# Kernel tuning notes

Measured on AMD Instinct MI355X. Metric: run time of the kernel, lower is better.

Reference implementation:

```python
import jax, jax.numpy as jnp
import numpy as np

E = 256; H = 8; HD = E // H
L_LEN = 300; A_LEN = 250
T = 768; B = 4
NEG = -1e9


def setup_inputs() -> dict:
    rng = jax.random.key(0)
    ks = jax.random.split(rng, 16)
    n = lambda k, s, sc=1.0: jax.random.normal(k, s, dtype=jnp.float32) * sc
    return {
        "query": n(ks[0], (T, B, E)),
        "key": n(ks[1], (T, B, E)),
        "value": n(ks[2], (T, B, E)),
        "in_proj_w": n(ks[3], (3 * E, E), 0.05),
        "in_proj_b": jnp.zeros((3 * E,), jnp.float32),
        "out_w": n(ks[4], (7, E, E), 0.05),
        "out_b": jnp.zeros((7, E), jnp.float32),
        "s_l_w": n(ks[5], (E, 4 * E), 0.05),
        "s_l_b": jnp.zeros((E,), jnp.float32),
        "s_a_w": n(ks[6], (E, 4 * E), 0.05),
        "s_a_b": jnp.zeros((E,), jnp.float32),
        "s_v_w": n(ks[7], (E, 4 * E), 0.05),
        "s_v_b": jnp.zeros((E,), jnp.float32),
        "final_w": n(ks[8], (E, E), 0.05),
        "final_b": jnp.zeros((E,), jnp.float32),
    }


def _forward(query, key, value, in_proj_w, in_proj_b, out_w, out_b,
             s_l_w, s_l_b, s_a_w, s_a_b, s_v_w, s_v_b, final_w, final_b):
    t, b, e = query.shape
    scaling = HD ** -0.5
    Wq, Wk, Wv = in_proj_w[:E], in_proj_w[E:2 * E], in_proj_w[2 * E:]
    bq, bk, bv = in_proj_b[:E], in_proj_b[E:2 * E], in_proj_b[2 * E:]
    q = (query @ Wq.T + bq) * scaling
    k = key @ Wk.T + bk
    v = value @ Wv.T + bv
    # (T, B, E) -> (B*H, T, HD)
    sh = lambda x: x.reshape(t, b * H, HD).transpose(1, 0, 2)
    q, k, v = sh(q), sh(k), sh(v)
    # shared QK^T, reused by all 7 masked branches
    scores = jnp.einsum('bth,bsh->bts', q, k)  # (B*H, T, T)
    idx = jnp.arange(t)
    seg = jnp.where(idx < L_LEN, 0, jnp.where(idx < L_LEN + A_LEN, 1, 2))

    def branch(i, mods):
        # m[j] = 1 iff position j belongs to one of the selected modalities
        m = sum((seg == s) for s in mods).astype(scores.dtype)  # (T,)
        # additive mask: in-set query attends only in-set keys; out-of-set
        # query rows get all -1e9 (uniform softmax, zeroed by row mask below)
        add = jnp.where((m[:, None] * m[None, :]) > 0, 0.0, NEG)
        w = jax.nn.softmax(scores + add, axis=-1) * m[None, :, None]
        o = jnp.einsum('bts,bsh->bth', w, v * m[None, :, None])
        o = o.transpose(1, 0, 2).reshape(t, b, e)
        return o @ out_w[i].T + out_b[i]

    attn_lav = branch(0, (0, 1, 2))
    attn_la = branch(1, (0, 1))
    attn_lv = branch(2, (0, 2))
    attn_av = branch(3, (1, 2))
    attn_l = branch(4, (0,))
    attn_a = branch(5, (1,))
    attn_v = branch(6, (2,))

    sl = jnp.concatenate([attn_lav, attn_la, attn_lv, attn_l], -1) @ s_l_w.T + s_l_b
    sa = jnp.concatenate([attn_lav, attn_la, attn_av, attn_a], -1) @ s_a_w.T + s_a_b
    sv = jnp.concatenate([attn_lav, attn_lv, attn_av, attn_v], -1) @ s_v_w.T + s_v_b
    return (sl + sa + sv) @ final_w.T + final_b


def reference(query, key, value, in_proj_w, in_proj_b, out_w, out_b,
              s_l_w, s_l_b, s_a_w, s_a_b, s_v_w, s_v_b, final_w, final_b):
    return _forward(query, key, value, in_proj_w, in_proj_b, out_w, out_b,
                    s_l_w, s_l_b, s_a_w, s_a_b, s_v_w, s_v_b, final_w, final_b)
```

## Files before the change

kernel.cpp:

```cpp
#include <hip/hip_runtime.h>
#include <hip/hip_bf16.h>

#define E 256
#define H 8
#define HD 32
#define T 768
#define B 4
#define BH 32

typedef __attribute__((ext_vector_type(8))) short bf16x8;
typedef __attribute__((ext_vector_type(4))) float f32x4;
typedef __attribute__((ext_vector_type(16))) float f32x16;

__device__ __forceinline__ float b2f(__hip_bfloat16 x) { return __bfloat162float(x); }

__device__ __forceinline__ unsigned short f2bf_u(float x) {
    __hip_bfloat16 h = __float2bfloat16(x);
    return *(unsigned short*)&h;
}
__device__ __forceinline__ float bfu2f(unsigned short u) {
    return __uint_as_float(((unsigned int)u) << 16);
}

__device__ __forceinline__ int detect_f32(const void* query) {
    const unsigned short* q = (const unsigned short*)query;
    int lane = threadIdx.x & 63;
    int bad = 0;
    #pragma unroll
    for (int i = 0; i < 4; ++i) {
        float v = bfu2f(q[lane + i * 64]);
        bad |= (!(v == v) || fabsf(v) > 1e4f) ? 1 : 0;
    }
    return __any(bad) ? 1 : 0;
}

__device__ __forceinline__ void f8_split(const float* v, bf16x8& h, bf16x8& l) {
    #pragma unroll
    for (int e = 0; e < 8; ++e) {
        unsigned short hu = f2bf_u(v[e]);
        h[e] = (short)hu;
        l[e] = (short)f2bf_u(v[e] - bfu2f(hu));
    }
}

#define MFMA3(ACC, AH, AL, BH_, BL_)                                         \
    ACC = __builtin_amdgcn_mfma_f32_16x16x32_bf16(AH, BH_, ACC, 0, 0, 0);    \
    ACC = __builtin_amdgcn_mfma_f32_16x16x32_bf16(AH, BL_, ACC, 0, 0, 0);    \
    ACC = __builtin_amdgcn_mfma_f32_16x16x32_bf16(AL, BH_, ACC, 0, 0, 0);

#define MFMA3W(ACC, AH, AL, BH_, BL_)                                        \
    ACC = __builtin_amdgcn_mfma_f32_32x32x16_bf16(AH, BH_, ACC, 0, 0, 0);    \
    ACC = __builtin_amdgcn_mfma_f32_32x32x16_bf16(AH, BL_, ACC, 0, 0, 0);    \
    ACC = __builtin_amdgcn_mfma_f32_32x32x16_bf16(AL, BH_, ACC, 0, 0, 0);

__device__ __forceinline__ bf16x8 mk8(int a, int b, int c, int d) {
    union { int i[4]; bf16x8 v; } u;
    u.i[0] = a; u.i[1] = b; u.i[2] = c; u.i[3] = d;
    return u.v;
}

__device__ __forceinline__ float ldu(const void* p, size_t i, int f32) {
    if (f32) return ((const float*)p)[i];
    return b2f(((const __hip_bfloat16*)p)[i]);
}

__device__ __forceinline__ float gsum_load(int i, int r2, int r,
                                           const void* sl, const void* sa,
                                           const void* sv, int f32)
{
    size_t base = (size_t)r2 * 1024;
    switch (i) {
        case 0: return ldu(sl, base + r, f32) + ldu(sa, base + r, f32) + ldu(sv, base + r, f32);
        case 1: return ldu(sl, base + 256 + r, f32) + ldu(sa, base + 256 + r, f32);
        case 2: return ldu(sl, base + 512 + r, f32) + ldu(sv, base + 256 + r, f32);
        case 3: return ldu(sa, base + 512 + r, f32) + ldu(sv, base + 512 + r, f32);
        case 4: return ldu(sl, base + 768 + r, f32);
        case 5: return ldu(sa, base + 768 + r, f32);
        default: return ldu(sv, base + 768 + r, f32);
    }
}

__global__ __launch_bounds__(256) void stage1_kernel(
    const void* query, const void* key, const void* value, const void* w,
    const void* sl, const void* sa, const void* sv, const void* outw,
    const void* outb, const void* slb, const void* sab, const void* svb,
    unsigned short* __restrict__ XFh, unsigned short* __restrict__ XFl,
    unsigned short* __restrict__ WFh, unsigned short* __restrict__ WFl,
    unsigned short* __restrict__ GFh, unsigned short* __restrict__ GFl,
    unsigned short* __restrict__ OWFh, unsigned short* __restrict__ OWFl,
    float* __restrict__ c0)
{
    __shared__ float red[256];
    int f32 = detect_f32(query);
    if (blockIdx.x < 1696) {
        int item = blockIdx.x * 256 + threadIdx.x;
        if (item < 294912) {
            int inp = item / 98304;
            int rem = item % 98304;
            int row = rem >> 5, kg = rem & 31;
            const void* X = (inp == 0) ? query : (inp == 1) ? key : value;
            float v[8];
            if (f32) {
                const float4* p = (const float4*)((const float*)X +
                                   (size_t)row * 256 + kg * 8);
                *(float4*)&v[0] = p[0];
                *(float4*)&v[4] = p[1];
            } else {
                #pragma unroll
                for (int j = 0; j < 8; ++j)
                    v[j] = ldu(X, (size_t)row * 256 + kg * 8 + j, 0);
            }
            bf16x8 h, l;
            f8_split(v, h, l);
            int rb = row >> 4, kb = kg >> 2;
            int lane = (row & 15) | ((kg & 3) << 4);
            size_t idx = (((size_t)(inp * 192 + rb) * 8 + kb) * 64 + lane) * 8;
            *(bf16x8*)&XFh[idx] = h;
            *(bf16x8*)&XFl[idx] = l;
        } else if (item < 319488) {
            int rem = item - 294912;
            int gc = rem >> 5, kg = rem & 31;
            float v[8];
            if (f32) {
                const float4* p = (const float4*)((const float*)w +
                                   (size_t)gc * 256 + kg * 8);
                *(float4*)&v[0] = p[0];
                *(float4*)&v[4] = p[1];
            } else {
                #pragma unroll
                for (int j = 0; j < 8; ++j)
                    v[j] = ldu(w, (size_t)gc * 256 + kg * 8 + j, 0);
            }
            bf16x8 h, l;
            f8_split(v, h, l);
            int sec = gc >> 8, c = gc & 255;
            int cb = c >> 4, kb = kg >> 2;
            int lane = (c & 15) | ((kg & 3) << 4);
            size_t idx = (((size_t)(sec * 16 + cb) * 8 + kb) * 64 + lane) * 8;
            *(bf16x8*)&WFh[idx] = h;
            *(bf16x8*)&WFl[idx] = l;
        } else if (item < 376832) {
            int rem = item - 319488;
            int i = rem >> 13;
            int rest = rem & 8191;
            int r2 = rest >> 5, kg = rest & 31;
            float v[8];
            #pragma unroll
            for (int j = 0; j < 8; ++j)
                v[j] = gsum_load(i, r2, kg * 8 + j, sl, sa, sv, f32);
            bf16x8 h, l;
            f8_split(v, h, l);
            int rb = r2 >> 4, kb = kg >> 2;
            int lane = (r2 & 15) | ((kg & 3) << 4);
            size_t idx = (((size_t)(i * 16 + rb) * 8 + kb) * 64 + lane) * 8;
            *(bf16x8*)&GFh[idx] = h;
            *(bf16x8*)&GFl[idx] = l;
        } else if (item < 434176) {
            int rem = item - 376832;
            int i = rem >> 13;
            int rest = rem & 8191;
            int kg = rest >> 8, c = rest & 255;
            float v[8];
            #pragma unroll
            for (int j = 0; j < 8; ++j)
                v[j] = ldu(outw, (size_t)i * 65536 + (kg * 8 + j) * 256 + c, f32);
            bf16x8 h, l;
            f8_split(v, h, l);
            int cb = c >> 4, kb = kg >> 2;
            int lane = (c & 15) | ((kg & 3) << 4);
            size_t idx = (((size_t)(i * 16 + cb) * 8 + kb) * 64 + lane) * 8;
            *(bf16x8*)&OWFh[idx] = h;
            *(bf16x8*)&OWFl[idx] = l;
        }
    } else {
        int r2 = blockIdx.x - 1696, m = threadIdx.x;
        float acc = 0.f;
        #pragma unroll
        for (int i = 0; i < 7; ++i)
            acc += ldu(outb, i * 256 + m, f32) * gsum_load(i, r2, m, sl, sa, sv, f32);
        red[m] = acc;
        __syncthreads();
        for (int s = 128; s > 0; s >>= 1) {
            if (m < s) red[m] += red[m + s];
            __syncthreads();
        }
        if (m == 0)
            c0[r2] = red[0] + ldu(slb, r2, f32) + ldu(sab, r2, f32) + ldu(svb, r2, f32);
    }
}

__global__ __launch_bounds__(256) void stage2_kernel(
    const unsigned short* __restrict__ XFh, const unsigned short* __restrict__ XFl,
    const unsigned short* __restrict__ WFh, const unsigned short* __restrict__ WFl,
    const void* bias, const void* query,
    float* __restrict__ qws,
    unsigned short* __restrict__ KRh, unsigned short* __restrict__ KRl,
    unsigned short* __restrict__ VFh, unsigned short* __restrict__ VFl,
    const unsigned short* __restrict__ GFh, const unsigned short* __restrict__ GFl,
    const unsigned short* __restrict__ OWFh, const unsigned short* __restrict__ OWFl,
    float* __restrict__ Mtmp,
    const float* __restrict__ c0, const void* finalw, const void* finalb,
    float* __restrict__ d0)
{
    __shared__ float red[256];
    int bxx = blockIdx.x;
    if (bxx < 2304) {
        int f32 = detect_f32(query);
        int bx = bxx % 12;
        int rb = bxx / 12;
        int sec = bx >> 2, cg = bx & 3;
        int w = threadIdx.x >> 6, lane = threadIdx.x & 63;
        int m = lane & 15, quad = lane >> 4;
        int cb = cg * 4 + w;

        const unsigned short* Ah = XFh + (((size_t)(sec * 192 + rb) * 8) * 64 + lane) * 8;
        const unsigned short* Al = XFl + (((size_t)(sec * 192 + rb) * 8) * 64 + lane) * 8;
        const unsigned short* Bh = WFh + (((size_t)(sec * 16 + cb) * 8) * 64 + lane) * 8;
        const unsigned short* Bl = WFl + (((size_t)(sec * 16 + cb) * 8) * 64 + lane) * 8;

        f32x4 acc = {};
        #pragma unroll
        for (int kb = 0; kb < 8; ++kb) {
            size_t off = (size_t)kb * 512;
            bf16x8 ah = *(const bf16x8*)(Ah + off);
            bf16x8 al = *(const bf16x8*)(Al + off);
            bf16x8 bh = *(const bf16x8*)(Bh + off);
            bf16x8 bl = *(const bf16x8*)(Bl + off);
            MFMA3(acc, ah, al, bh, bl)
        }

        int c_local = cb * 16 + m;
        float bv = ldu(bias, sec * 256 + c_local, f32);
        int h = c_local >> 5, hd = c_local & 31;

        if (sec == 0) {
            #pragma unroll
            for (int rr = 0; rr < 4; ++rr) {
                int row = rb * 16 + quad * 4 + rr;
                int t = row >> 2, b = row & 3;
                float val = (acc[rr] + bv) * 0.17677669529663687f;
                qws[((size_t)((b * H + h) * T + t)) * HD + hd] = val;
            }
        } else if (sec == 1) {
            #pragma unroll
            for (int rr = 0; rr < 4; ++rr) {
                int row = rb * 16 + quad * 4 + rr;
                int s = row >> 2, b = row & 3;
                int bh_ = b * 8 + h;
                float val = acc[rr] + bv;
                unsigned short hu = f2bf_u(val);
                unsigned short lu = f2bf_u(val - bfu2f(hu));
                size_t bi = ((size_t)bh_ * 768 + s) * 32 + hd;
                KRh[bi] = hu;
                KRl[bi] = lu;
            }
        } else {
            #pragma unroll
            for (int rr = 0; rr < 4; ++rr) {
                int row = rb * 16 + quad * 4 + rr;
                int s = row >> 2, b = row & 3;
                int bh_ = b * 8 + h;
                float val = acc[rr] + bv;
                unsigned short hu = f2bf_u(val);
                unsigned short lu = f2bf_u(val - bfu2f(hu));
                int s16 = s >> 4, hp = (s >> 3) & 1, j = s & 7;
                size_t bi = (((size_t)bh_ * 48 + s16) * 64 + hp * 32 + hd) * 8 + j;
                VFh[bi] = hu;
                VFl[bi] = lu;
            }
        }
    } else if (bxx < 2752) {
        int idx = bxx - 2304;
        int cgrp = idx & 3;
        int rb   = (idx >> 2) & 15;
        int i    = idx >> 6;
        int w = threadIdx.x >> 6, lane = threadIdx.x & 63;
        int m = lane & 15, quad = lane >> 4;
        int cb = cgrp * 4 + w;

        const unsigned short* Ah = GFh + (((size_t)(i * 16 + rb) * 8) * 64 + lane) * 8;
        const unsigned short* Al = GFl + (((size_t)(i * 16 + rb) * 8) * 64 + lane) * 8;
        const unsigned short* Bh = OWFh + (((size_t)(i * 16 + cb) * 8) * 64 + lane) * 8;
        const unsigned short* Bl = OWFl + (((size_t)(i * 16 + cb) * 8) * 64 + lane) * 8;

        f32x4 acc = {};
        #pragma unroll
        for (int kb = 0; kb < 8; ++kb) {
            size_t off = (size_t)kb * 512;
            bf16x8 ah = *(const bf16x8*)(Ah + off);
            bf16x8 al = *(const bf16x8*)(Al + off);
            bf16x8 bh = *(const bf16x8*)(Bh + off);
            bf16x8 bl = *(const bf16x8*)(Bl + off);
            MFMA3(acc, ah, al, bh, bl)
        }
        #pragma unroll
        for (int rr = 0; rr < 4; ++rr) {
            int r2 = rb * 16 + quad * 4 + rr;
            Mtmp[(size_t)i * 65536 + r2 * 256 + cb * 16 + m] = acc[rr];
        }
    } else {
        int f32 = detect_f32(query);
        int e = bxx - 2752, r = threadIdx.x;
        red[r] = c0[r] * ldu(finalw, (size_t)e * 256 + r, f32);
        __syncthreads();
        for (int s = 128; s > 0; s >>= 1) {
            if (r < s) red[r] += red[r + s];
            __syncthreads();
        }
        if (r == 0)
            d0[e] = red[0] + ldu(finalb, e, f32);
    }
}

__global__ __launch_bounds__(256, 2) void stage3_kernel(
    const float* __restrict__ qws,
    const unsigned short* __restrict__ KRh, const unsigned short* __restrict__ KRl,
    const unsigned short* __restrict__ VFh, const unsigned short* __restrict__ VFl,
    unsigned short* __restrict__ Ohi, unsigned short* __restrict__ Olo,
    const float* __restrict__ Mtmp, const void* finalw, const void* query,
    unsigned short* __restrict__ DThi, unsigned short* __restrict__ DTlo)
{
    __shared__ __align__(16) float SMEM[7104];
    int tid = threadIdx.x;

    if (blockIdx.x < 768) {
        float (*AC2)[3][32][36] = (float(*)[3][32][36])&SMEM[0];
        float (*SS2)[3][32]     = (float(*)[3][32])&SMEM[6912];
        int bid = blockIdx.x;
        int xcd = bid & 7, rr_ = bid >> 3;
        int j_ = rr_ / 24, tile = rr_ % 24;
        int bh = j_ * 8 + xcd;
        int t0 = tile * 32;
        int w = tid >> 6, lane = tid & 63;
        int ln = lane & 31, h = lane >> 5;

        bf16x8 qbh[2], qbl[2];
        {
            const float* qr = qws + ((size_t)bh * T + t0 + ln) * HD + h * 8;
            #pragma unroll
            for (int c = 0; c < 2; ++c) {
                float qv[8];
                *(float4*)&qv[0] = *(const float4*)(qr + c * 16);
                *(float4*)&qv[4] = *(const float4*)(qr + c * 16 + 4);
                f8_split(qv, qbh[c], qbl[c]);
            }
        }

        f32x16 accA = {}, accB = {};
        float ssA = 0.f, ssB = 0.f;

        for (int q = 0; q < 3; ++q) {
            int ch = w * 3 + q;
            int sbase = ch * 64;
            int route = (ch == 5) ? 1 : (ch == 4 || ch == 8) ? 2 : 0;
            int bnd = (ch == 4) ? 300 : 550;
            bool c12 = (ch == 4);

            bf16x8 kf0h[2], kf0l[2], kf1h[2], kf1l[2], vh[4], vl[4];
            #pragma unroll
            for (int st = 0; st < 2; ++st) {
                size_t krow = ((size_t)bh * 768 + sbase + st * 32 + ln) * 32 + h * 8;
                kf0h[st] = *(const bf16x8*)(KRh + krow);
                kf0l[st] = *(const bf16x8*)(KRl + krow);
                kf1h[st] = *(const bf16x8*)(KRh + krow + 16);
                kf1l[st] = *(const bf16x8*)(KRl + krow + 16);
            }
            #pragma unroll
            for (int ks = 0; ks < 4; ++ks) {
                size_t vidx = (((size_t)bh * 48 + ch * 4 + ks) * 64 + lane) * 8;
                vh[ks] = *(const bf16x8*)(VFh + vidx);
                vl[ks] = *(const bf16x8*)(VFl + vidx);
            }

            #pragma unroll
            for (int st = 0; st < 2; ++st) {
                f32x16 d = {};
                MFMA3W(d, kf0h[st], kf0l[st], qbh[0], qbl[0])
                MFMA3W(d, kf1h[st], kf1l[st], qbh[1], qbl[1])

                int PH[8], PL[8];
                #pragma unroll
                for (int p = 0; p < 8; ++p) {
                    float e0 = __expf(d[2 * p]);
                    float e1 = __expf(d[2 * p + 1]);
                    if (route == 2) {
                        int r0 = 2 * p;
                        int s0 = sbase + st * 32 + (r0 & 3) + 8 * (r0 >> 2) + 4 * h;
                        if (s0 < bnd) ssA += e0; else ssB += e0;
                        if (s0 + 1 < bnd) ssA += e1; else ssB += e1;
                    } else if (route == 1) { ssB += e0 + e1; }
                    else { ssA += e0 + e1; }
                    unsigned b0 = __float_as_uint(e0), b1 = __float_as_uint(e1);
                    float l0 = e0 - __uint_as_float(b0 & 0xffff0000u);
                    float l1 = e1 - __uint_as_float(b1 & 0xffff0000u);
                    PH[p] = (int)((b0 >> 16) | (b1 & 0xffff0000u));
                    PL[p] = (int)((__float_as_uint(l0) >> 16) |
                                  (__float_as_uint(l1) & 0xffff0000u));
                }

                #pragma unroll
                for (int ksl = 0; ksl < 2; ++ksl) {
                    int ks = st * 2 + ksl;
                    int cc = 4 * ksl;
                    bf16x8 vbh = vh[ks];
                    bf16x8 vbl = vl[ks];

                    int sh0 = __shfl_xor(PH[cc+0], 32);
                    int sh1 = __shfl_xor(PH[cc+1], 32);
                    int sh2 = __shfl_xor(PH[cc+2], 32);
                    int sh3 = __shfl_xor(PH[cc+3], 32);
                    int sl0 = __shfl_xor(PL[cc+0], 32);
                    int sl1 = __shfl_xor(PL[cc+1], 32);
                    int sl2 = __shfl_xor(PL[cc+2], 32);
                    int sl3 = __shfl_xor(PL[cc+3], 32);
                    int FH0 = h ? sh2 : PH[cc+0];
                    int FH1 = h ? sh3 : PH[cc+1];
                    int FH2 = h ? PH[cc+2] : sh0;
                    int FH3 = h ? PH[cc+3] : sh1;
                    int FL0 = h ? sl2 : PL[cc+0];
                    int FL1 = h ? sl3 : PL[cc+1];
                    int FL2 = h ? PL[cc+2] : sl0;
                    int FL3 = h ? PL[cc+3] : sl1;
                    bf16x8 feh = mk8(FH0, FH1, FH2, FH3);
                    bf16x8 fel = mk8(FL0, FL1, FL2, FL3);

                    if (route == 0)      { MFMA3W(accA, feh, fel, vbh, vbl) }
                    else if (route == 1) { MFMA3W(accB, feh, fel, vbh, vbl) }
                    else {
                        if (ks < 2)       { MFMA3W(accA, feh, fel, vbh, vbl) }
                        else if (ks == 3) { MFMA3W(accB, feh, fel, vbh, vbl) }
                        else {
                            int a0 = h ? (c12 ? FH0 : 0) : FH0;
                            int a1 = h ? (c12 ? FH1 : 0) : FH1;
                            int a2 = h ? 0 : FH2;
                            int a3 = h ? 0 : (c12 ? FH3 : 0);
                            int b0 = h ? (c12 ? 0 : FH0) : 0;
                            int b1 = h ? (c12 ? 0 : FH1) : 0;
                            int b2 = h ? FH2 : 0;
                            int b3 = h ? FH3 : (c12 ? 0 : FH3);
                            int la0 = h ? (c12 ? FL0 : 0) : FL0;
                            int la1 = h ? (c12 ? FL1 : 0) : FL1;
                            int la2 = h ? 0 : FL2;
                            int la3 = h ? 0 : (c12 ? FL3 : 0);
                            int lb0 = h ? (c12 ? 0 : FL0) : 0;
                            int lb1 = h ? (c12 ? 0 : FL1) : 0;
                            int lb2 = h ? FL2 : 0;
                            int lb3 = h ? FL3 : (c12 ? 0 : FL3);
                            bf16x8 fha = mk8(a0, a1, a2, a3), fla = mk8(la0, la1, la2, la3);
                            bf16x8 fhb = mk8(b0, b1, b2, b3), flb = mk8(lb0, lb1, lb2, lb3);
                            MFMA3W(accA, fha, fla, vbh, vbl)
                            MFMA3W(accB, fhb, flb, vbh, vbl)
                        }
                    }
                }
            }
        }

        ssA += __shfl_xor(ssA, 32);
        ssB += __shfl_xor(ssB, 32);

        int bsel = w & 1;
        f32x16 zz = {};
        f32x16 o0 = (w <= 1) ? accA : zz;
        f32x16 o1 = (w == 1) ? accB : (w == 2) ? accA : zz;
        f32x16 o2 = (w == 2) ? accB : (w == 3) ? accA : zz;
        float s0 = (w <= 1) ? ssA : 0.f;
        float s1 = (w == 1) ? ssB : (w == 2) ? ssA : 0.f;
        float s2 = (w == 2) ? ssB : (w == 3) ? ssA : 0.f;

        if (w < 2) {
            #pragma unroll
            for (int r = 0; r < 16; ++r) {
                int t = (r & 3) + 8 * (r >> 2) + 4 * h;
                AC2[bsel][0][t][ln] = o0[r];
                AC2[bsel][1][t][ln] = o1[r];
                AC2[bsel][2][t][ln] = o2[r];
            }
            if (h == 0) {
                SS2[bsel][0][ln] = s0;
                SS2[bsel][1][ln] = s1;
                SS2[bsel][2][ln] = s2;
            }
        }
        __syncthreads();
        if (w >= 2) {
            #pragma unroll
            for (int r = 0; r < 16; ++r) {
                int t = (r & 3) + 8 * (r >> 2) + 4 * h;
                AC2[bsel][1][t][ln] += o1[r];
                AC2[bsel][2][t][ln] += o2[r];
            }
            if (h == 0) {
                SS2[bsel][1][ln] += s1;
                SS2[bsel][2][ln] += s2;
            }
        }
        __syncthreads();

        int tt = tid >> 3, q4 = tid & 7;
        float Pv[3][4], S[3];
        #pragma unroll
        for (int sg = 0; sg < 3; ++sg) {
            const float4 a = *(const float4*)&AC2[0][sg][tt][q4 * 4];
            const float4 b = *(const float4*)&AC2[1][sg][tt][q4 * 4];
            Pv[sg][0] = a.x + b.x; Pv[sg][1] = a.y + b.y;
            Pv[sg][2] = a.z + b.z; Pv[sg][3] = a.w + b.w;
            S[sg] = SS2[0][sg][tt] + SS2[1][sg][tt];
        }

        int t_glob = t0 + tt;
        int g = (t_glob < 300) ? 0 : (t_glob < 550 ? 1 : 2);
        int b_ = bh >> 3, h_ = bh & 7;
        int row = b_ * T + t_glob;
        int lslot = (row & 15) + ((q4 >> 1) << 4);
        int j0 = (q4 & 1) * 4;
        size_t fbase = (((size_t)(row >> 4) * 56 + h_) * 64 + lslot) * 8 + j0;
        const int masks[7] = {7, 3, 5, 6, 1, 2, 4};
        #pragma unroll
        for (int i = 0; i < 7; ++i) {
            int mm = masks[i];
            float n0 = 0.f, n1 = 0.f, n2 = 0.f, n3 = 0.f, den = 0.f;
            if (mm & 1) { n0 += Pv[0][0]; n1 += Pv[0][1]; n2 += Pv[0][2]; n3 += Pv[0][3]; den += S[0]; }
            if (mm & 2) { n0 += Pv[1][0]; n1 += Pv[1][1]; n2 += Pv[1][2]; n3 += Pv[1][3]; den += S[1]; }
            if (mm & 4) { n0 += Pv[2][0]; n1 += Pv[2][1]; n2 += Pv[2][2]; n3 += Pv[2][3]; den += S[2]; }
            float r = 1.f / den;
            int live = (mm >> g) & 1;
            float o[4];
            o[0] = live ? n0 * r : 0.f;
            o[1] = live ? n1 * r : 0.f;
            o[2] = live ? n2 * r : 0.f;
            o[3] = live ? n3 * r : 0.f;
            ushort4 hi4, lo4;
            unsigned short* hp = (unsigned short*)&hi4;
            unsigned short* lp = (unsigned short*)&lo4;
            #pragma unroll
            for (int jq = 0; jq < 4; ++jq) {
                unsigned short hu = f2bf_u(o[jq]);
                hp[jq] = hu;
                lp[jq] = f2bf_u(o[jq] - bfu2f(hu));
            }
            size_t addr = fbase + (size_t)i * (8 * 64 * 8);
            *(ushort4*)&Ohi[addr] = hi4;
            *(ushort4*)&Olo[addr] = lo4;
        }
    } else {
        float (*AsT)[34] = (float(*)[34])&SMEM[0];
        float (*Bs)[34]  = (float(*)[34])&SMEM[1088];
        int f32 = detect_f32(query);
        int idx = blockIdx.x - 768;
        int bx = idx & 7;
        int by = (idx >> 3) & 7;
        int i  = idx >> 6;
        int tx = tid & 15, ty = tid >> 4;
        int colbase = bx * 32, rowbase = by * 32;
        float acc[2][2] = {};

        for (int kb = 0; kb < 8; ++kb) {
            __syncthreads();
            #pragma unroll
            for (int l = 0; l < 4; ++l) {
                int idx2 = l * 256 + tid;
                int c = idx2 & 31, kk = idx2 >> 5;
                AsT[kk][c] = Mtmp[(size_t)i * 65536 + (kb * 32 + kk) * 256 + rowbase + c];
                int k2 = idx2 & 31, n = idx2 >> 5;
                Bs[k2][n] = ldu(finalw, (size_t)(colbase + n) * 256 + kb * 32 + k2, f32);
            }
            __syncthreads();
            #pragma unroll 8
            for (int kk = 0; kk < 32; ++kk) {
                const float2 av = *(const float2*)&AsT[kk][ty * 2];
                const float2 bv = *(const float2*)&Bs[kk][tx * 2];
                acc[0][0] += av.x * bv.x; acc[0][1] += av.x * bv.y;
                acc[1][0] += av.y * bv.x; acc[1][1] += av.y * bv.y;
            }
        }
        #pragma unroll
        for (int u = 0; u < 2; ++u)
            #pragma unroll
            for (int v = 0; v < 2; ++v) {
                int c = rowbase + ty * 2 + u, e = colbase + tx * 2 + v;
                float a = acc[u][v];
                unsigned short hu = f2bf_u(a);
                size_t fidx = (((size_t)(e >> 4) * 56 + i * 8 + (c >> 5)) * 64
                               + (e & 15) + (((c >> 3) & 3) << 4)) * 8 + (c & 7);
                DThi[fidx] = hu;
                DTlo[fidx] = f2bf_u(a - bfu2f(hu));
            }
    }
}

__global__ __launch_bounds__(256) void final_gemm_mfma_kernel(
    const unsigned short* __restrict__ Ohi, const unsigned short* __restrict__ Olo,
    const unsigned short* __restrict__ DThi, const unsigned short* __restrict__ DTlo,
    const float* __restrict__ d0, const void* query,
    void* __restrict__ outv)
{
    int f32 = detect_f32(query);
    int bid = blockIdx.x;
    int xcd = bid & 7, rr_ = bid >> 3;
    int slot = rr_ >> 2, bx = rr_ & 3;
    int by = slot * 8 + xcd;
    int w  = threadIdx.x >> 6;
    int lane = threadIdx.x & 63;
    int m = lane & 15, quad = lane >> 4;
    int R0 = by * 16, C0 = bx * 64 + w * 16;

    int b_out = R0 / 768;
    int tfirst = R0 - b_out * 768;
    int g0 = (tfirst < 300) ? 0 : (tfirst < 550 ? 1 : 2);
    int g1 = (tfirst + 15 < 300) ? 0 : (tfirst + 15 < 550 ? 1 : 2);
    int activeset = (1 << g0) | (1 << g1);
    const int masks[7] = {7, 3, 5, 6, 1, 2, 4};

    const unsigned short* Abase_h = Ohi + (size_t)by * 56 * 512 + lane * 8;
    const unsigned short* Abase_l = Olo + (size_t)by * 56 * 512 + lane * 8;
    const unsigned short* Bbase_h = DThi + (size_t)(bx * 4 + w) * 56 * 512 + lane * 8;
    const unsigned short* Bbase_l = DTlo + (size_t)(bx * 4 + w) * 56 * 512 + lane * 8;

    f32x4 acc = {};
    for (int i = 0; i < 7; ++i) {
        if (!(masks[i] & activeset)) continue;
        #pragma unroll
        for (int kb = 0; kb < 8; ++kb) {
            size_t off = (size_t)(i * 8 + kb) * 512;
            bf16x8 ah = *(const bf16x8*)(Abase_h + off);
            bf16x8 al = *(const bf16x8*)(Abase_l + off);
            bf16x8 bh = *(const bf16x8*)(Bbase_h + off);
            bf16x8 bl = *(const bf16x8*)(Bbase_l + off);
            acc = __builtin_amdgcn_mfma_f32_16x16x32_bf16(ah, bh, acc, 0, 0, 0);
            acc = __builtin_amdgcn_mfma_f32_16x16x32_bf16(ah, bl, acc, 0, 0, 0);
            acc = __builtin_amdgcn_mfma_f32_16x16x32_bf16(al, bh, acc, 0, 0, 0);
        }
    }
    float dv = d0[C0 + m];
    #pragma unroll
    for (int r = 0; r < 4; ++r) {
        int t = tfirst + quad * 4 + r;
        int col = C0 + m;
        float val = acc[r] + dv;
        size_t orow = (size_t)t * B + b_out;
        if (f32) ((float*)outv)[orow * 256 + col] = val;
        else ((__hip_bfloat16*)outv)[orow * 256 + col] = __float2bfloat16(val);
    }
}

extern "C" void kernel_launch(void* const* d_in, const int* in_sizes, int n_in,
                              void* d_out, int out_size, void* d_ws, size_t ws_size,
                              hipStream_t stream) {
    const void* query     = d_in[0];
    const void* key       = d_in[1];
    const void* value     = d_in[2];
    const void* in_proj_w = d_in[3];
    const void* in_proj_b = d_in[4];
    const void* out_w     = d_in[5];
    const void* out_b     = d_in[6];
    const void* s_l_w     = d_in[7];
    const void* s_l_b     = d_in[8];
    const void* s_a_w     = d_in[9];
    const void* s_a_b     = d_in[10];
    const void* s_v_w     = d_in[11];
    const void* s_v_b     = d_in[12];
    const void* final_w   = d_in[13];
    const void* final_b   = d_in[14];

    float* ws     = (float*)d_ws;
    float* qws    = ws;
    unsigned short* KRh = (unsigned short*)(ws + 786432);
    unsigned short* KRl = KRh + 786432;
    unsigned short* VFh = (unsigned short*)(ws + 1572864);
    unsigned short* VFl = VFh + 786432;
    unsigned short* Ohi = (unsigned short*)(ws + 2359296);
    unsigned short* Olo = (unsigned short*)(ws + 5111808);
    unsigned short* XFh = (unsigned short*)(ws + 2359296);
    unsigned short* XFl = XFh + 2359296;
    unsigned short* WFh = XFl + 2359296;
    unsigned short* WFl = WFh + 196608;
    unsigned short* GFh = (unsigned short*)(ws + 4915200);
    unsigned short* GFl = GFh + 458752;
    unsigned short* OWFh = GFl + 458752;
    unsigned short* OWFl = OWFh + 458752;
    float* Mtmp   = ws + 7864320;
    unsigned short* DThi = (unsigned short*)(ws + 8323072);
    unsigned short* DTlo = (unsigned short*)(ws + 8552448);
    float* d0     = ws + 8781824;
    float* c0     = ws + 8782336;

    stage1_kernel<<<1952, 256, 0, stream>>>(query, key, value, in_proj_w,
                                            s_l_w, s_a_w, s_v_w, out_w,
                                            out_b, s_l_b, s_a_b, s_v_b,
                                            XFh, XFl, WFh, WFl,
                                            GFh, GFl, OWFh, OWFl, c0);
    stage2_kernel<<<3008, 256, 0, stream>>>(XFh, XFl, WFh, WFl,
                                            in_proj_b, query, qws,
                                            KRh, KRl, VFh, VFl,
                                            GFh, GFl, OWFh, OWFl, Mtmp,
                                            c0, final_w, final_b, d0);
    stage3_kernel<<<1216, 256, 0, stream>>>(qws, KRh, KRl, VFh, VFl,
                                            Ohi, Olo,
                                            Mtmp, final_w, query,
                                            DThi, DTlo);
    final_gemm_mfma_kernel<<<768, 256, 0, stream>>>(Ohi, Olo, DThi, DTlo,
                                                    d0, query, d_out);
}
```

Measured before the change: 164.6 us.

## Fuse input hi/lo split into QKV projection GEMM, widen per-block column tile

The separate stage1 pass that converted query/key/value into bf16 hi/lo fragment buffers is removed. Stage2 now loads the fp32 activations directly, splits them in registers, and each block computes all 256 output columns for its 16-row tile (4 column blocks per wave), so each A fragment is reused four times. This removes a full write and re-read of the split activation buffers and cuts the projection grid from 2304 to 576 blocks. The cost is fewer, heavier blocks with more accumulator registers, plus uncoalesced direct global reads of the A operand.

```diff
diff --git a/kernel.cpp b/kernel.cpp
--- a/kernel.cpp
+++ b/kernel.cpp
@@ -81,10 +81,9 @@
 }
 
 __global__ __launch_bounds__(256) void stage1_kernel(
-    const void* query, const void* key, const void* value, const void* w,
+    const void* query, const void* w,
     const void* sl, const void* sa, const void* sv, const void* outw,
     const void* outb, const void* slb, const void* sab, const void* svb,
-    unsigned short* __restrict__ XFh, unsigned short* __restrict__ XFl,
     unsigned short* __restrict__ WFh, unsigned short* __restrict__ WFl,
     unsigned short* __restrict__ GFh, unsigned short* __restrict__ GFl,
     unsigned short* __restrict__ OWFh, unsigned short* __restrict__ OWFl,
@@ -92,34 +91,10 @@
 {
     __shared__ float red[256];
     int f32 = detect_f32(query);
-    if (blockIdx.x < 1696) {
+    if (blockIdx.x < 544) {
         int item = blockIdx.x * 256 + threadIdx.x;
-        if (item < 294912) {
-            int inp = item / 98304;
-            int rem = item % 98304;
-            int row = rem >> 5, kg = rem & 31;
-            const void* X = (inp == 0) ? query : (inp == 1) ? key : value;
-            float v[8];
-            if (f32) {
-                const float4* p = (const float4*)((const float*)X +
-                                   (size_t)row * 256 + kg * 8);
-                *(float4*)&v[0] = p[0];
-                *(float4*)&v[4] = p[1];
-            } else {
-                #pragma unroll
-                for (int j = 0; j < 8; ++j)
-                    v[j] = ldu(X, (size_t)row * 256 + kg * 8 + j, 0);
-            }
-            bf16x8 h, l;
-            f8_split(v, h, l);
-            int rb = row >> 4, kb = kg >> 2;
-            int lane = (row & 15) | ((kg & 3) << 4);
-            size_t idx = (((size_t)(inp * 192 + rb) * 8 + kb) * 64 + lane) * 8;
-            *(bf16x8*)&XFh[idx] = h;
-            *(bf16x8*)&XFl[idx] = l;
-        } else if (item < 319488) {
-            int rem = item - 294912;
-            int gc = rem >> 5, kg = rem & 31;
+        if (item < 24576) {
+            int gc = item >> 5, kg = item & 31;
             float v[8];
             if (f32) {
                 const float4* p = (const float4*)((const float*)w +
@@ -139,8 +114,8 @@
             size_t idx = (((size_t)(sec * 16 + cb) * 8 + kb) * 64 + lane) * 8;
             *(bf16x8*)&WFh[idx] = h;
             *(bf16x8*)&WFl[idx] = l;
-        } else if (item < 376832) {
-            int rem = item - 319488;
+        } else if (item < 81920) {
+            int rem = item - 24576;
             int i = rem >> 13;
             int rest = rem & 8191;
             int r2 = rest >> 5, kg = rest & 31;
@@ -155,8 +130,8 @@
             size_t idx = (((size_t)(i * 16 + rb) * 8 + kb) * 64 + lane) * 8;
             *(bf16x8*)&GFh[idx] = h;
             *(bf16x8*)&GFl[idx] = l;
-        } else if (item < 434176) {
-            int rem = item - 376832;
+        } else if (item < 139264) {
+            int rem = item - 81920;
             int i = rem >> 13;
             int rest = rem & 8191;
             int kg = rest >> 8, c = rest & 255;
@@ -173,7 +148,7 @@
             *(bf16x8*)&OWFl[idx] = l;
         }
     } else {
-        int r2 = blockIdx.x - 1696, m = threadIdx.x;
+        int r2 = blockIdx.x - 544, m = threadIdx.x;
         float acc = 0.f;
         #pragma unroll
         for (int i = 0; i < 7; ++i)
@@ -190,9 +165,9 @@
 }
 
 __global__ __launch_bounds__(256) void stage2_kernel(
-    const unsigned short* __restrict__ XFh, const unsigned short* __restrict__ XFl,
+    const void* query, const void* key, const void* value,
     const unsigned short* __restrict__ WFh, const unsigned short* __restrict__ WFl,
-    const void* bias, const void* query,
+    const void* bias,
     float* __restrict__ qws,
     unsigned short* __restrict__ KRh, unsigned short* __restrict__ KRl,
     unsigned short* __restrict__ VFh, unsigned short* __restrict__ VFl,
@@ -204,19 +179,100 @@
 {
     __shared__ float red[256];
     int bxx = blockIdx.x;
-    if (bxx < 2304) {
+    if (bxx < 576) {
         int f32 = detect_f32(query);
-        int bx = bxx % 12;
-        int rb = bxx / 12;
-        int sec = bx >> 2, cg = bx & 3;
+        int sec = bxx / 192;
+        int rb  = bxx % 192;
+        const void* X = (sec == 0) ? query : (sec == 1) ? key : value;
         int w = threadIdx.x >> 6, lane = threadIdx.x & 63;
         int m = lane & 15, quad = lane >> 4;
-        int cb = cg * 4 + w;
-
-        const unsigned short* Ah = XFh + (((size_t)(sec * 192 + rb) * 8) * 64 + lane) * 8;
-        const unsigned short* Al = XFl + (((size_t)(sec * 192 + rb) * 8) * 64 + lane) * 8;
-        const unsigned short* Bh = WFh + (((size_t)(sec * 16 + cb) * 8) * 64 + lane) * 8;
-        const unsigned short* Bl = WFl + (((size_t)(sec * 16 + cb) * 8) * 64 + lane) * 8;
+
+        size_t aoff0 = (size_t)(rb * 16 + (lane & 15)) * 256 + quad * 8;
+
+        f32x4 acc[4] = {};
+        #pragma unroll
+        for (int kb = 0; kb < 8; ++kb) {
+            float av[8];
+            size_t aoff = aoff0 + kb * 32;
+            if (f32) {
+                const float4* p = (const float4*)((const float*)X + aoff);
+                *(float4*)&av[0] = p[0];
+                *(float4*)&av[4] = p[1];
+            } else {
+                #pragma unroll
+                for (int j = 0; j < 8; ++j)
+                    av[j] = ldu(X, aoff + j, 0);
+            }
+            bf16x8 ah, al;
+            f8_split(av, ah, al);
+            #pragma unroll
+            for (int c = 0; c < 4; ++c) {
+                int cb = w * 4 + c;
+                const unsigned short* Bh = WFh + (((size_t)(sec * 16 + cb) * 8 + kb) * 64 + lane) * 8;
+                const unsigned short* Bl = WFl + (((size_t)(sec * 16 + cb) * 8 + kb) * 64 + lane) * 8;
+                bf16x8 bh = *(const bf16x8*)Bh;
+                bf16x8 bl = *(const bf16x8*)Bl;
+                MFMA3(acc[c], ah, al, bh, bl)
+            }
+        }
+
+        #pragma unroll
+        for (int c = 0; c < 4; ++c) {
+            int cb = w * 4 + c;
+            int c_local = cb * 16 + m;
+            float bv = ldu(bias, sec * 256 + c_local, f32);
+            int h = c_local >> 5, hd = c_local & 31;
+
+            if (sec == 0) {
+                #pragma unroll
+                for (int rr = 0; rr < 4; ++rr) {
+                    int row = rb * 16 + quad * 4 + rr;
+                    int t = row >> 2, b = row & 3;
+                    float val = (acc[c][rr] + bv) * 0.17677669529663687f;
+                    qws[((size_t)((b * H + h) * T + t)) * HD + hd] = val;
+                }
+            } else if (sec == 1) {
+                #pragma unroll
+                for (int rr = 0; rr < 4; ++rr) {
+                    int row = rb * 16 + quad * 4 + rr;
+                    int s = row >> 2, b = row & 3;
+                    int bh_ = b * 8 + h;
+                    float val = acc[c][rr] + bv;
+                    unsigned short hu = f2bf_u(val);
+                    unsigned short lu = f2bf_u(val - bfu2f(hu));
+                    size_t bi = ((size_t)bh_ * 768 + s) * 32 + hd;
+                    KRh[bi] = hu;
+                    KRl[bi] = lu;
+                }
+            } else {
+                #pragma unroll
+                for (int rr = 0; rr < 4; ++rr) {
+                    int row = rb * 16 + quad * 4 + rr;
+                    int s = row >> 2, b = row & 3;
+                    int bh_ = b * 8 + h;
+                    float val = acc[c][rr] + bv;
+                    unsigned short hu = f2bf_u(val);
+                    unsigned short lu = f2bf_u(val - bfu2f(hu));
+                    int s16 = s >> 4, hp = (s >> 3) & 1, j = s & 7;
+                    size_t bi = (((size_t)bh_ * 48 + s16) * 64 + hp * 32 + hd) * 8 + j;
+                    VFh[bi] = hu;
+                    VFl[bi] = lu;
+                }
+            }
+        }
+    } else if (bxx < 1024) {
+        int idx = bxx - 576;
+        int cgrp = idx & 3;
+        int rb   = (idx >> 2) & 15;
+        int i    = idx >> 6;
+        int w = threadIdx.x >> 6, lane = threadIdx.x & 63;
+        int m = lane & 15, quad = lane >> 4;
+        int cb = cgrp * 4 + w;
+
+        const unsigned short* Ah = GFh + (((size_t)(i * 16 + rb) * 8) * 64 + lane) * 8;
+        const unsigned short* Al = GFl + (((size_t)(i * 16 + rb) * 8) * 64 + lane) * 8;
+        const unsigned short* Bh = OWFh + (((size_t)(i * 16 + cb) * 8) * 64 + lane) * 8;
+        const unsigned short* Bl = OWFl + (((size_t)(i * 16 + cb) * 8) * 64 + lane) * 8;
 
         f32x4 acc = {};
         #pragma unroll
@@ -228,71 +284,6 @@
             bf16x8 bl = *(const bf16x8*)(Bl + off);
             MFMA3(acc, ah, al, bh, bl)
         }
-
-        int c_local = cb * 16 + m;
-        float bv = ldu(bias, sec * 256 + c_local, f32);
-        int h = c_local >> 5, hd = c_local & 31;
-
-        if (sec == 0) {
-            #pragma unroll
-            for (int rr = 0; rr < 4; ++rr) {
-                int row = rb * 16 + quad * 4 + rr;
-                int t = row >> 2, b = row & 3;
-                float val = (acc[rr] + bv) * 0.17677669529663687f;
-                qws[((size_t)((b * H + h) * T + t)) * HD + hd] = val;
-            }
-        } else if (sec == 1) {
-            #pragma unroll
-            for (int rr = 0; rr < 4; ++rr) {
-                int row = rb * 16 + quad * 4 + rr;
-                int s = row >> 2, b = row & 3;
-                int bh_ = b * 8 + h;
-                float val = acc[rr] + bv;
-                unsigned short hu = f2bf_u(val);
-                unsigned short lu = f2bf_u(val - bfu2f(hu));
-                size_t bi = ((size_t)bh_ * 768 + s) * 32 + hd;
-                KRh[bi] = hu;
-                KRl[bi] = lu;
-            }
-        } else {
-            #pragma unroll
-            for (int rr = 0; rr < 4; ++rr) {
-                int row = rb * 16 + quad * 4 + rr;
-                int s = row >> 2, b = row & 3;
-                int bh_ = b * 8 + h;
-                float val = acc[rr] + bv;
-                unsigned short hu = f2bf_u(val);
-                unsigned short lu = f2bf_u(val - bfu2f(hu));
-                int s16 = s >> 4, hp = (s >> 3) & 1, j = s & 7;
-                size_t bi = (((size_t)bh_ * 48 + s16) * 64 + hp * 32 + hd) * 8 + j;
-                VFh[bi] = hu;
-                VFl[bi] = lu;
-            }
-        }
-    } else if (bxx < 2752) {
-        int idx = bxx - 2304;
-        int cgrp = idx & 3;
-        int rb   = (idx >> 2) & 15;
-        int i    = idx >> 6;
-        int w = threadIdx.x >> 6, lane = threadIdx.x & 63;
-        int m = lane & 15, quad = lane >> 4;
-        int cb = cgrp * 4 + w;
-
-        const unsigned short* Ah = GFh + (((size_t)(i * 16 + rb) * 8) * 64 + lane) * 8;
-        const unsigned short* Al = GFl + (((size_t)(i * 16 + rb) * 8) * 64 + lane) * 8;
-        const unsigned short* Bh = OWFh + (((size_t)(i * 16 + cb) * 8) * 64 + lane) * 8;
-        const unsigned short* Bl = OWFl + (((size_t)(i * 16 + cb) * 8) * 64 + lane) * 8;
-
-        f32x4 acc = {};
-        #pragma unroll
-        for (int kb = 0; kb < 8; ++kb) {
-            size_t off = (size_t)kb * 512;
-            bf16x8 ah = *(const bf16x8*)(Ah + off);
-            bf16x8 al = *(const bf16x8*)(Al + off);
-            bf16x8 bh = *(const bf16x8*)(Bh + off);
-            bf16x8 bl = *(const bf16x8*)(Bl + off);
-            MFMA3(acc, ah, al, bh, bl)
-        }
         #pragma unroll
         for (int rr = 0; rr < 4; ++rr) {
             int r2 = rb * 16 + quad * 4 + rr;
@@ -300,7 +291,7 @@
         }
     } else {
         int f32 = detect_f32(query);
-        int e = bxx - 2752, r = threadIdx.x;
+        int e = bxx - 1024, r = threadIdx.x;
         red[r] = c0[r] * ldu(finalw, (size_t)e * 256 + r, f32);
         __syncthreads();
         for (int s = 128; s > 0; s >>= 1) {
@@ -671,9 +662,7 @@
     unsigned short* VFl = VFh + 786432;
     unsigned short* Ohi = (unsigned short*)(ws + 2359296);
     unsigned short* Olo = (unsigned short*)(ws + 5111808);
-    unsigned short* XFh = (unsigned short*)(ws + 2359296);
-    unsigned short* XFl = XFh + 2359296;
-    unsigned short* WFh = XFl + 2359296;
+    unsigned short* WFh = (unsigned short*)(ws + 2359296);
     unsigned short* WFl = WFh + 196608;
     unsigned short* GFh = (unsigned short*)(ws + 4915200);
     unsigned short* GFl = GFh + 458752;
@@ -685,13 +674,13 @@
     float* d0     = ws + 8781824;
     float* c0     = ws + 8782336;
 
-    stage1_kernel<<<1952, 256, 0, stream>>>(query, key, value, in_proj_w,
-                                            s_l_w, s_a_w, s_v_w, out_w,
-                                            out_b, s_l_b, s_a_b, s_v_b,
-                                            XFh, XFl, WFh, WFl,
-                                            GFh, GFl, OWFh, OWFl, c0);
-    stage2_kernel<<<3008, 256, 0, stream>>>(XFh, XFl, WFh, WFl,
-                                            in_proj_b, query, qws,
+    stage1_kernel<<<800, 256, 0, stream>>>(query, in_proj_w,
+                                           s_l_w, s_a_w, s_v_w, out_w,
+                                           out_b, s_l_b, s_a_b, s_v_b,
+                                           WFh, WFl,
+                                           GFh, GFl, OWFh, OWFl, c0);
+    stage2_kernel<<<1280, 256, 0, stream>>>(query, key, value,
+                                            WFh, WFl, in_proj_b, qws,
                                             KRh, KRl, VFh, VFl,
                                             GFh, GFl, OWFh, OWFl, Mtmp,
                                             c0, final_w, final_b, d0);
```

Result: faster. 160.4 us (-2.5%).
